# Kernel optimization log

Hardware: AMD Instinct MI355X
Metric: run time of the kernel (lower is better)

## Reference

```python
import jax, jax.numpy as jnp
import numpy as np

SEQ, B, IN, H, L = 256, 512, 300, 512, 256
EPS = 1e-5


def setup_inputs() -> dict:
    key = jax.random.key(0)
    ks = jax.random.split(key, 10)
    s_ih = 1.0 / np.sqrt(H)
    return {
        "x": jax.random.normal(ks[0], (SEQ, B, IN), dtype=jnp.float32),
        "W_ih": jax.random.normal(ks[1], (4 * H, IN), dtype=jnp.float32) * s_ih,
        "W_hh": jax.random.normal(ks[2], (4 * H, H), dtype=jnp.float32) * s_ih,
        "b_ih": jax.random.normal(ks[3], (4 * H,), dtype=jnp.float32) * s_ih,
        "b_hh": jax.random.normal(ks[4], (4 * H,), dtype=jnp.float32) * s_ih,
        "bn1_gamma": jnp.ones((H,), dtype=jnp.float32),
        "bn1_beta": jnp.zeros((H,), dtype=jnp.float32),
        "W1": jax.random.normal(ks[5], (L, H), dtype=jnp.float32) / np.sqrt(H),
        "b1": jax.random.normal(ks[6], (L,), dtype=jnp.float32) * 0.01,
        "bn2_gamma": jnp.ones((L,), dtype=jnp.float32),
        "bn2_beta": jnp.zeros((L,), dtype=jnp.float32),
        "W2": jax.random.normal(ks[7], (1, L), dtype=jnp.float32) / np.sqrt(L),
        "b2": jax.random.normal(ks[8], (1,), dtype=jnp.float32) * 0.01,
    }


def _batchnorm(x, gamma, beta):
    # training-mode BatchNorm1d: batch statistics, biased variance
    mean = jnp.mean(x, axis=0)
    var = jnp.var(x, axis=0)
    return (x - mean) * jax.lax.rsqrt(var + EPS) * gamma + beta


def reference(x, W_ih, W_hh, b_ih, b_hh, bn1_gamma, bn1_beta, W1, b1,
              bn2_gamma, bn2_beta, W2, b2):
    # Pre-compute the input projection for all timesteps in one big GEMM:
    # [S, B, IN] @ [IN, 4H] -> [S, B, 4H]
    x_proj = jnp.einsum('sbi,gi->sbg', x, W_ih) + b_ih + b_hh

    def step(carry, xt):
        h, c = carry
        gates = xt + h @ W_hh.T  # [B, 4H]
        i, f, g, o = jnp.split(gates, 4, axis=-1)
        i = jax.nn.sigmoid(i)
        f = jax.nn.sigmoid(f)
        g = jnp.tanh(g)
        o = jax.nn.sigmoid(o)
        c = f * c + i * g
        h = o * jnp.tanh(c)
        return (h, c), None

    h0 = jnp.zeros((x.shape[1], H), dtype=x.dtype)
    c0 = jnp.zeros((x.shape[1], H), dtype=x.dtype)
    (h, _c), _ = jax.lax.scan(step, (h0, c0), x_proj)
    # dropout with training=False -> identity

    h = _batchnorm(h, bn1_gamma, bn1_beta)
    h = h @ W1.T + b1
    h = _batchnorm(h, bn2_gamma, bn2_beta)
    h = jax.nn.relu(h)
    out = h @ W2.T + b2            # [B, 1]
    out = 4.0 * jax.nn.sigmoid(out)
    return out.squeeze(-1)         # [B]
```

## Files before the change

kernel.cpp:

```cpp
#include <hip/hip_runtime.h>
#include <math.h>

constexpr int SEQ   = 256;
constexpr int BATCH = 512;
constexpr int INDIM = 300;
constexpr int KIH   = 320;
constexpr int HDIM  = 512;
constexpr int LDIM  = 256;
constexpr int G4    = 4 * HDIM;

typedef _Float16 f16x8 __attribute__((ext_vector_type(8)));
typedef _Float16 f16x4 __attribute__((ext_vector_type(4)));
typedef float    f32x4 __attribute__((ext_vector_type(4)));


__global__ __launch_bounds__(256) void prep_weights_kernel(
    const float* __restrict__ Wih, const float* __restrict__ Whh,
    const float* __restrict__ bih, const float* __restrict__ bhh,
    _Float16* __restrict__ slab, float* __restrict__ bsum)
{
    const int by = blockIdx.x >> 6;
    const int rl = blockIdx.x & 63;
    const int g  = rl >> 4, r = rl & 15;
    const int grow = g * HDIM + by * 16 + r;
    const int tid = threadIdx.x;
    if (tid < 208) {
        const int col0 = tid * 4;
        f16x4 v;
        #pragma unroll
        for (int e = 0; e < 4; ++e) {
            const int col = col0 + e;
            float f;
            if (col < KIH) f = (col < INDIM) ? Wih[(size_t)grow * INDIM + col] : 0.f;
            else           f = Whh[(size_t)grow * HDIM + (col - KIH)];
            v[e] = (_Float16)f;
        }
        *(f16x4*)(slab + ((size_t)(by * 64 + rl)) * 832 + col0) = v;
    } else if (tid == 208) {
        bsum[grow] = bih[grow] + bhh[grow];
    }
}

__global__ __launch_bounds__(256) void prep_x_kernel(
    const float* __restrict__ x, _Float16* __restrict__ xall)
{
    const int rowl = threadIdx.x >> 6;
    const int s    = threadIdx.x & 63;
    const int row  = blockIdx.x * 4 + rowl;
    if (s >= 40) return;
    const int k0 = s * 8;
    const float* xr = x + (size_t)row * INDIM;
    f16x8 v;
    #pragma unroll
    for (int e = 0; e < 8; ++e)
        v[e] = (k0 + e < INDIM) ? (_Float16)xr[k0 + e] : (_Float16)0.f;
    *(f16x8*)(xall + (size_t)row * KIH + k0) = v;
}

__global__ __launch_bounds__(512, 2) void lstm_persist11(
    const _Float16* __restrict__ xall,
    const _Float16* __restrict__ slab,
    _Float16* __restrict__ hb,
    float* __restrict__ h32,
    const float* __restrict__ bsum,
    int* __restrict__ cnt)
{
    __shared__ _Float16 act[13][64][64];
    __shared__ float    Gb2[2][64][68];

    const int tid  = threadIdx.x;
    const int wid  = tid >> 6;
    const int lane = tid & 63;
    const int gg   = wid >> 2;
    const int bh   = (wid >> 1) & 1;
    const int ks   = wid & 1;
    const int l15  = lane & 15;
    const int q4   = lane >> 4;
    const int bx   = blockIdx.x & 7;
    const int by   = blockIdx.x >> 3;
    const int b0   = bx * 64;
    const int hc0  = by * 16;

    f16x8 ws[13][2];
    {
        const _Float16* sb = slab + (size_t)by * 64 * 832
                                  + (size_t)(gg * 32 + l15) * 832 + ks * 32 + q4 * 8;
        #pragma unroll
        for (int ch = 0; ch < 13; ++ch)
            #pragma unroll
            for (int mt = 0; mt < 2; ++mt) {
                const unsigned long long* p = (const unsigned long long*)
                    (sb + (size_t)mt * 16 * 832 + ch * 64);
                union { unsigned long long u[2]; f16x8 v; } w;
                w.u[0] = __hip_atomic_load(p,     __ATOMIC_RELAXED,
                                           __HIP_MEMORY_SCOPE_AGENT);
                w.u[1] = __hip_atomic_load(p + 1, __ATOMIC_RELAXED,
                                           __HIP_MEMORY_SCOPE_AGENT);
                ws[ch][mt] = w.v;
            }
    }

    const int srow  = tid >> 3;
    const int suu   = tid & 7;
    const int wbyte = srow * 128 + ((suu ^ (srow & 7)) << 4);

    int rbyte[2];
    #pragma unroll
    for (int bt = 0; bt < 2; ++bt) {
        const int row  = bh * 32 + bt * 16 + l15;
        const int unit = ks * 4 + q4;
        rbyte[bt] = row * 128 + ((unit ^ (row & 7)) << 4);
    }

    const int bl  = tid >> 3;
    const int j0l = (tid & 7) * 2;
    const int bg  = b0 + bl;
    const int jg  = hc0 + j0l;
    float bsv[4][2];
    #pragma unroll
    for (int g = 0; g < 4; ++g) {
        bsv[g][0] = bsum[g * HDIM + jg];
        bsv[g][1] = bsum[g * HDIM + jg + 1];
    }
    float cv0 = 0.f, cv1 = 0.f;

#define BARX() do { asm volatile("" ::: "memory");                           \
                    __builtin_amdgcn_s_barrier();                            \
                    asm volatile("" ::: "memory"); } while (0)
#define LGKM0() asm volatile("s_waitcnt lgkmcnt(0)" ::: "memory")
#define VM0()   asm volatile("s_waitcnt vmcnt(0)" ::: "memory")

#define MFMA_CHUNK(CH) do {                                                  \
        const char* base = (const char*)&act[CH][0][0];                      \
        const f16x8 bf0 = *(const f16x8*)(base + rbyte[0]);                  \
        const f16x8 bf1 = *(const f16x8*)(base + rbyte[1]);                  \
        acc00 = __builtin_amdgcn_mfma_f32_16x16x32_f16(ws[CH][0], bf0, acc00, 0, 0, 0); \
        acc01 = __builtin_amdgcn_mfma_f32_16x16x32_f16(ws[CH][0], bf1, acc01, 0, 0, 0); \
        acc10 = __builtin_amdgcn_mfma_f32_16x16x32_f16(ws[CH][1], bf0, acc10, 0, 0, 0); \
        acc11 = __builtin_amdgcn_mfma_f32_16x16x32_f16(ws[CH][1], bf1, acc11, 0, 0, 0); \
    } while (0)

    const _Float16* xpt = xall + (size_t)(b0 + srow) * KIH + suu * 8;
    const _Float16* hpt = hb + (size_t)(b0 + srow) * HDIM + suu * 8;

    f16x8 xcur[5], xnxt[5];
    #pragma unroll
    for (int ch = 0; ch < 5; ++ch)
        xcur[ch] = *(const f16x8*)(xpt + ch * 64);

    for (int t = 0; t < SEQ; ++t) {
        #pragma unroll
        for (int ch = 0; ch < 5; ++ch)
            *(f16x8*)((char*)&act[ch][0][0] + wbyte) = xcur[ch];
        LGKM0(); BARX();

        f32x4 acc00 = {0.f,0.f,0.f,0.f}, acc01 = {0.f,0.f,0.f,0.f};
        f32x4 acc10 = {0.f,0.f,0.f,0.f}, acc11 = {0.f,0.f,0.f,0.f};

        if (wid == 0) {
            if (t > 0) {
                const int* fp = cnt + bx * 32 + (lane & 31);
                int wd = 0;
                for (;;) {
                    const int f = __hip_atomic_load(fp, __ATOMIC_RELAXED,
                                                    __HIP_MEMORY_SCOPE_AGENT);
                    if (__all(f >= t)) break;
                    if (++wd > (1 << 20)) break;
                    __builtin_amdgcn_s_sleep(2);
                }
                asm volatile("" ::: "memory");
            }
        } else {
            MFMA_CHUNK(0); MFMA_CHUNK(1); MFMA_CHUNK(2);
            MFMA_CHUNK(3); MFMA_CHUNK(4);
        }
        BARX();

        f16x8 hr[8];
        {
            const _Float16* hbase = hpt + (size_t)(t & 1) * BATCH * HDIM;
            #pragma unroll
            for (int j = 0; j < 8; ++j) {
                const unsigned long long* p = (const unsigned long long*)
                    (hbase + j * 64);
                union { unsigned long long u[2]; f16x8 v; } hv;
                hv.u[0] = __hip_atomic_load(p,     __ATOMIC_RELAXED,
                                            __HIP_MEMORY_SCOPE_AGENT);
                hv.u[1] = __hip_atomic_load(p + 1, __ATOMIC_RELAXED,
                                            __HIP_MEMORY_SCOPE_AGENT);
                hr[j] = hv.v;
            }
        }
        if (wid == 0) {
            MFMA_CHUNK(0); MFMA_CHUNK(1); MFMA_CHUNK(2);
            MFMA_CHUNK(3); MFMA_CHUNK(4);
        }
        {
            const _Float16* xnb = xpt + (size_t)(t + 1) * BATCH * KIH;
            #pragma unroll
            for (int ch = 0; ch < 5; ++ch)
                xnxt[ch] = *(const f16x8*)(xnb + ch * 64);
        }
        #pragma unroll
        for (int j = 0; j < 8; ++j)
            *(f16x8*)((char*)&act[5 + j][0][0] + wbyte) = hr[j];
        LGKM0(); BARX();

        MFMA_CHUNK(5); MFMA_CHUNK(6); MFMA_CHUNK(7); MFMA_CHUNK(8);
        MFMA_CHUNK(9); MFMA_CHUNK(10); MFMA_CHUNK(11); MFMA_CHUNK(12);

        #pragma unroll
        for (int q = 0; q < 4; ++q) {
            Gb2[ks][gg * 32 +      q4 * 4 + q][bh * 32 +      l15] = acc00[q];
            Gb2[ks][gg * 32 +      q4 * 4 + q][bh * 32 + 16 + l15] = acc01[q];
            Gb2[ks][gg * 32 + 16 + q4 * 4 + q][bh * 32 +      l15] = acc10[q];
            Gb2[ks][gg * 32 + 16 + q4 * 4 + q][bh * 32 + 16 + l15] = acc11[q];
        }
        LGKM0(); BARX();

        {
            float pre[4][2];
            #pragma unroll
            for (int g = 0; g < 4; ++g) {
                pre[g][0] = Gb2[0][g * 16 + j0l    ][bl]
                          + Gb2[1][g * 16 + j0l    ][bl] + bsv[g][0];
                pre[g][1] = Gb2[0][g * 16 + j0l + 1][bl]
                          + Gb2[1][g * 16 + j0l + 1][bl] + bsv[g][1];
            }
            float hv0, hv1;
            {
                float vi = 1.f / (1.f + __expf(-pre[0][0]));
                float vf = 1.f / (1.f + __expf(-pre[1][0]));
                float vg = 1.f - 2.f / (__expf(2.f * pre[2][0]) + 1.f);
                float vo = 1.f / (1.f + __expf(-pre[3][0]));
                const float cc = vf * cv0 + vi * vg;
                cv0 = cc;
                hv0 = vo * (1.f - 2.f / (__expf(2.f * cc) + 1.f));
            }
            {
                float vi = 1.f / (1.f + __expf(-pre[0][1]));
                float vf = 1.f / (1.f + __expf(-pre[1][1]));
                float vg = 1.f - 2.f / (__expf(2.f * pre[2][1]) + 1.f);
                float vo = 1.f / (1.f + __expf(-pre[3][1]));
                const float cc = vf * cv1 + vi * vg;
                cv1 = cc;
                hv1 = vo * (1.f - 2.f / (__expf(2.f * cc) + 1.f));
            }
            union { unsigned int u; _Float16 v[2]; } hu;
            hu.v[0] = (_Float16)hv0; hu.v[1] = (_Float16)hv1;
            _Float16* hbw = hb + (size_t)((t + 1) & 1) * BATCH * HDIM;
            __hip_atomic_store((unsigned int*)(hbw + (size_t)bg * HDIM + jg),
                               hu.u, __ATOMIC_RELAXED, __HIP_MEMORY_SCOPE_AGENT);
            if (t == SEQ - 1) {
                float* hp = h32 + (size_t)bg * HDIM + jg;
                hp[0] = hv0; hp[1] = hv1;
            }
        }
        VM0(); BARX();
        if (tid == 0)
            __hip_atomic_store(&cnt[bx * 32 + by], t + 1, __ATOMIC_RELAXED,
                               __HIP_MEMORY_SCOPE_AGENT);

        #pragma unroll
        for (int ch = 0; ch < 5; ++ch) xcur[ch] = xnxt[ch];
    }
#undef BARX
#undef LGKM0
#undef VM0
#undef MFMA_CHUNK
}

__global__ __launch_bounds__(256) void prep_kernel(
    const float* __restrict__ Wih, const float* __restrict__ Whh,
    const float* __restrict__ bih, const float* __restrict__ bhh,
    _Float16* __restrict__ Wihc, _Float16* __restrict__ Whhc,
    float* __restrict__ bsum)
{
    const int g = blockIdx.x;
    for (int col = threadIdx.x; col < KIH; col += 256)
        Wihc[(size_t)g * KIH + col] =
            (col < INDIM) ? (_Float16)Wih[(size_t)g * INDIM + col] : (_Float16)0.f;
    for (int col = threadIdx.x; col < HDIM; col += 256)
        Whhc[(size_t)g * HDIM + col] = (_Float16)Whh[(size_t)g * HDIM + col];
    if (threadIdx.x == 0) bsum[g] = bih[g] + bhh[g];
}

__global__ __launch_bounds__(256) void fused_step_kernel(
    const float* __restrict__ xt, const _Float16* __restrict__ Wihc,
    const _Float16* __restrict__ Whhc, const float* __restrict__ bsum,
    float* __restrict__ c, float* __restrict__ h)
{
    __shared__ _Float16 As[32][72];
    __shared__ _Float16 Bs[128][72];
    __shared__ float    Gb[4][32][36];

    const int tid = threadIdx.x;
    const int b0  = blockIdx.x * 32;
    const int hc0 = blockIdx.y * 32;
    const int wid  = tid >> 6;
    const int lane = tid & 63;

    f32x4 acc[2][2] = {};
    const int arow = tid >> 3;
    const int ac8  = (tid & 7) * 8;
    const int brr  = tid >> 1;
    const int bseg = (tid & 1) * 32;

    for (int phase = 0; phase < 2; ++phase) {
        const float* Asrc = phase ? h : xt;
        const _Float16* Bsrc = phase ? Whhc : Wihc;
        const int Kpad = phase ? HDIM : KIH;
        const int Kval = phase ? HDIM : INDIM;
        const int astr = phase ? HDIM : INDIM;

        for (int k0 = 0; k0 < Kpad; k0 += 64) {
            const int gk = k0 + ac8;
            const float* pa = Asrc + (size_t)(b0 + arow) * astr + gk;
            float4 u = {0.f,0.f,0.f,0.f}, v = {0.f,0.f,0.f,0.f};
            if (gk + 3 < Kval)  u = *(const float4*)pa;
            if (gk + 7 < Kval)  v = *(const float4*)(pa + 4);
            f16x8 a8;
            a8[0]=(_Float16)u.x; a8[1]=(_Float16)u.y; a8[2]=(_Float16)u.z; a8[3]=(_Float16)u.w;
            a8[4]=(_Float16)v.x; a8[5]=(_Float16)v.y; a8[6]=(_Float16)v.z; a8[7]=(_Float16)v.w;
            const int grow = (brr >> 5) * HDIM + hc0 + (brr & 31);
            const _Float16* pb = Bsrc + (size_t)grow * Kpad + k0 + bseg;
            f16x8 w0 = *(const f16x8*)(pb + 0);
            f16x8 w1 = *(const f16x8*)(pb + 8);
            f16x8 w2 = *(const f16x8*)(pb + 16);
            f16x8 w3 = *(const f16x8*)(pb + 24);
            __syncthreads();
            *(f16x8*)&As[arow][ac8] = a8;
            *(f16x8*)&Bs[brr][bseg + 0]  = w0;
            *(f16x8*)&Bs[brr][bseg + 8]  = w1;
            *(f16x8*)&Bs[brr][bseg + 16] = w2;
            *(f16x8*)&Bs[brr][bseg + 24] = w3;
            __syncthreads();
            const int lr = lane & 15;
            const int lk = (lane >> 4) * 8;
            #pragma unroll
            for (int kf = 0; kf < 2; ++kf) {
                const int kl = kf * 32 + lk;
                f16x8 a0 = *(const f16x8*)&As[lr][kl];
                f16x8 a1 = *(const f16x8*)&As[16 + lr][kl];
                f16x8 bb0 = *(const f16x8*)&Bs[wid * 32 + lr][kl];
                f16x8 bb1 = *(const f16x8*)&Bs[wid * 32 + 16 + lr][kl];
                acc[0][0] = __builtin_amdgcn_mfma_f32_16x16x32_f16(a0, bb0, acc[0][0], 0, 0, 0);
                acc[0][1] = __builtin_amdgcn_mfma_f32_16x16x32_f16(a0, bb1, acc[0][1], 0, 0, 0);
                acc[1][0] = __builtin_amdgcn_mfma_f32_16x16x32_f16(a1, bb0, acc[1][0], 0, 0, 0);
                acc[1][1] = __builtin_amdgcn_mfma_f32_16x16x32_f16(a1, bb1, acc[1][1], 0, 0, 0);
            }
        }
    }
    __syncthreads();
    {
        const int cn = lane & 15;
        const int rbq = (lane >> 4) * 4;
        #pragma unroll
        for (int mi = 0; mi < 2; ++mi)
            #pragma unroll
            for (int ni = 0; ni < 2; ++ni)
                #pragma unroll
                for (int r = 0; r < 4; ++r)
                    Gb[wid][mi * 16 + rbq + r][ni * 16 + cn] = acc[mi][ni][r];
    }
    __syncthreads();
    {
        const int bl  = tid >> 3;
        const int jl0 = (tid & 7) * 4;
        const int gb  = b0 + bl;
        const int gj  = hc0 + jl0;
        const f32x4 ig = *(const f32x4*)&Gb[0][bl][jl0];
        const f32x4 fg = *(const f32x4*)&Gb[1][bl][jl0];
        const f32x4 gg = *(const f32x4*)&Gb[2][bl][jl0];
        const f32x4 og = *(const f32x4*)&Gb[3][bl][jl0];
        const f32x4 bi = *(const f32x4*)&bsum[0 * HDIM + gj];
        const f32x4 bf = *(const f32x4*)&bsum[1 * HDIM + gj];
        const f32x4 bg = *(const f32x4*)&bsum[2 * HDIM + gj];
        const f32x4 bo = *(const f32x4*)&bsum[3 * HDIM + gj];
        float* cp = c + (size_t)gb * HDIM + gj;
        float* hp = h + (size_t)gb * HDIM + gj;
        f32x4 cvv = *(const f32x4*)cp;
        f32x4 hv;
        #pragma unroll
        for (int q = 0; q < 4; ++q) {
            const float iv = 1.f / (1.f + __expf(-(ig[q] + bi[q])));
            const float fv = 1.f / (1.f + __expf(-(fg[q] + bf[q])));
            const float gv = tanhf(gg[q] + bg[q]);
            const float ov = 1.f / (1.f + __expf(-(og[q] + bo[q])));
            const float cc = fv * cvv[q] + iv * gv;
            cvv[q] = cc;
            hv[q] = ov * tanhf(cc);
        }
        *(f32x4*)cp = cvv;
        *(f32x4*)hp = hv;
    }
}

__global__ __launch_bounds__(256) void bn_stats_kernel(
    const float* __restrict__ X, int nfeat,
    const float* __restrict__ gamma, const float* __restrict__ beta,
    float* __restrict__ s, float* __restrict__ t)
{
    const int f = blockIdx.x * 256 + threadIdx.x;
    if (f >= nfeat) return;
    float sum = 0.f, sq = 0.f;
    for (int b = 0; b < BATCH; ++b) {
        const float v = X[(size_t)b * nfeat + f];
        sum += v; sq += v * v;
    }
    const float mean = sum * (1.f / BATCH);
    const float var  = sq * (1.f / BATCH) - mean * mean;
    const float rstd = rsqrtf(var + 1e-5f);
    const float sc   = gamma[f] * rstd;
    s[f] = sc;
    t[f] = beta[f] - mean * sc;
}

__global__ __launch_bounds__(256) void fc1_kernel(
    const float* __restrict__ h, const float* __restrict__ s1,
    const float* __restrict__ t1, const float* __restrict__ W1,
    const float* __restrict__ b1, float* __restrict__ out1)
{
    const int b = blockIdx.x;
    const int l = threadIdx.x;
    const float* hbp = h  + (size_t)b * HDIM;
    const float* wl  = W1 + (size_t)l * HDIM;
    float acc = 0.f;
    for (int k = 0; k < HDIM; ++k)
        acc += (hbp[k] * s1[k] + t1[k]) * wl[k];
    out1[(size_t)b * LDIM + l] = acc + b1[l];
}

__global__ __launch_bounds__(256) void final_kernel(
    const float* __restrict__ out1, const float* __restrict__ s2,
    const float* __restrict__ t2, const float* __restrict__ W2,
    const float* __restrict__ b2, float* __restrict__ out)
{
    const int b = blockIdx.x;
    float v = out1[(size_t)b * LDIM + threadIdx.x];
    v = v * s2[threadIdx.x] + t2[threadIdx.x];
    v = fmaxf(v, 0.f);
    v *= W2[threadIdx.x];
    #pragma unroll
    for (int off = 32; off > 0; off >>= 1) v += __shfl_down(v, off);
    __shared__ float red[4];
    if ((threadIdx.x & 63) == 0) red[threadIdx.x >> 6] = v;
    __syncthreads();
    if (threadIdx.x == 0) {
        const float ssum = red[0] + red[1] + red[2] + red[3] + b2[0];
        out[b] = 4.f / (1.f + expf(-ssum));
    }
}

extern "C" void kernel_launch(void* const* d_in, const int* in_sizes, int n_in,
                              void* d_out, int out_size, void* d_ws, size_t ws_size,
                              hipStream_t stream) {
    const float* x   = (const float*)d_in[0];
    const float* Wih = (const float*)d_in[1];
    const float* Whh = (const float*)d_in[2];
    const float* bih = (const float*)d_in[3];
    const float* bhh = (const float*)d_in[4];
    const float* g1  = (const float*)d_in[5];
    const float* be1 = (const float*)d_in[6];
    const float* W1  = (const float*)d_in[7];
    const float* b1  = (const float*)d_in[8];
    const float* g2  = (const float*)d_in[9];
    const float* be2 = (const float*)d_in[10];
    const float* W2  = (const float*)d_in[11];
    const float* b2  = (const float*)d_in[12];
    float* out = (float*)d_out;

    const size_t SZ_XALL = (size_t)(SEQ + 1) * BATCH * KIH * 2;
    const size_t SZ_SLAB = (size_t)32 * 64 * 832 * 2;
    const size_t SZ_HB   = (size_t)2 * BATCH * HDIM * 2;
    const size_t SZ_H32  = (size_t)BATCH * HDIM * 4;
    const size_t SZ_BSUM = (size_t)G4 * 4;
    const size_t SZ_CNT  = (size_t)SEQ * 8 * 4;
    const size_t SZ_ST   = (size_t)(HDIM * 2 + LDIM * 2) * 4;
    const size_t SZ_OUT1 = (size_t)BATCH * LDIM * 4;
    const size_t NEED = SZ_XALL + SZ_SLAB + SZ_HB + SZ_H32 + SZ_BSUM +
                        SZ_CNT + SZ_ST + SZ_OUT1;

    if (ws_size >= NEED) {
        char* p = (char*)d_ws;
        _Float16* xall = (_Float16*)p;           p += SZ_XALL;
        _Float16* slab = (_Float16*)p;           p += SZ_SLAB;
        _Float16* hbuf = (_Float16*)p;           p += SZ_HB;
        float* h32     = (float*)p;              p += SZ_H32;
        float* bsum    = (float*)p;              p += SZ_BSUM;
        int*   cnt     = (int*)p;                p += SZ_CNT;
        float* s1 = (float*)p;                   p += HDIM * 4;
        float* t1 = (float*)p;                   p += HDIM * 4;
        float* s2 = (float*)p;                   p += LDIM * 4;
        float* t2 = (float*)p;                   p += LDIM * 4;
        float* out1 = (float*)p;

        hipMemsetAsync(hbuf, 0, SZ_HB, stream);
        hipMemsetAsync(cnt, 0, SZ_CNT, stream);
        prep_weights_kernel<<<2048, 256, 0, stream>>>(Wih, Whh, bih, bhh, slab, bsum);
        prep_x_kernel<<<SEQ * 128, 256, 0, stream>>>(x, xall);

        lstm_persist11<<<dim3(256), dim3(512), 0, stream>>>(
            xall, slab, hbuf, h32, bsum, cnt);

        bn_stats_kernel<<<2, 256, 0, stream>>>(h32, HDIM, g1, be1, s1, t1);
        fc1_kernel<<<BATCH, 256, 0, stream>>>(h32, s1, t1, W1, b1, out1);
        bn_stats_kernel<<<1, 256, 0, stream>>>(out1, LDIM, g2, be2, s2, t2);
        final_kernel<<<BATCH, 256, 0, stream>>>(out1, s2, t2, W2, b2, out);
    } else {
        float* ws   = (float*)d_ws;
        float* h    = ws;
        float* c    = h + BATCH * HDIM;
        float* bsum = c + BATCH * HDIM;
        float* s1   = bsum + G4;
        float* t1   = s1 + HDIM;
        float* s2   = t1 + HDIM;
        float* t2   = s2 + LDIM;
        float* out1 = t2 + LDIM;
        _Float16* Wihc = (_Float16*)(out1 + (size_t)BATCH * LDIM);
        _Float16* Whhc = Wihc + (size_t)G4 * KIH;

        hipMemsetAsync(h, 0, (size_t)2 * BATCH * HDIM * sizeof(float), stream);
        prep_kernel<<<G4, 256, 0, stream>>>(Wih, Whh, bih, bhh, Wihc, Whhc, bsum);
        const dim3 sgrid(BATCH / 32, HDIM / 32);
        for (int t = 0; t < SEQ; ++t) {
            fused_step_kernel<<<sgrid, 256, 0, stream>>>(
                x + (size_t)t * BATCH * INDIM, Wihc, Whhc, bsum, c, h);
        }
        bn_stats_kernel<<<2, 256, 0, stream>>>(h, HDIM, g1, be1, s1, t1);
        fc1_kernel<<<BATCH, 256, 0, stream>>>(h, s1, t1, W1, b1, out1);
        bn_stats_kernel<<<1, 256, 0, stream>>>(out1, LDIM, g2, be2, s2, t2);
        final_kernel<<<BATCH, 256, 0, stream>>>(out1, s2, t2, W2, b2, out);
    }
}
```

Measured before the change: 1.281 ms.

## Split recurrent h wait and load into four quarter-pipelined stages

Instead of one wave waiting on all 32 producer flags before any h load, every wave now waits on 8 flags at a time, loads and stages that quarter of h into shared memory, and runs MFMAs on the previous quarter while waiting for the next. The aim is to overlap the cross-block synchronisation latency with the recurrent matmul, so work can start as soon as part of h_t is published. The cost is more block barriers per step (four instead of two), all waves polling global flags, and a shorter sleep, which adds memory traffic and barrier overhead.

```diff
diff --git a/kernel.cpp b/kernel.cpp
--- a/kernel.cpp
+++ b/kernel.cpp
@@ -57,7 +57,7 @@
     *(f16x8*)(xall + (size_t)row * KIH + k0) = v;
 }
 
-__global__ __launch_bounds__(512, 2) void lstm_persist11(
+__global__ __launch_bounds__(512, 2) void lstm_persist12(
     const _Float16* __restrict__ xall,
     const _Float16* __restrict__ slab,
     _Float16* __restrict__ hb,
@@ -140,6 +140,40 @@
         acc11 = __builtin_amdgcn_mfma_f32_16x16x32_f16(ws[CH][1], bf1, acc11, 0, 0, 0); \
     } while (0)
 
+#define WAITQ(G) do {                                                        \
+    if (t > 0) {                                                             \
+        const int* fp = cnt + bx * 32 + (G) * 8 + (lane & 7);                \
+        int wd = 0;                                                          \
+        for (;;) {                                                           \
+            const int f = __hip_atomic_load(fp, __ATOMIC_RELAXED,            \
+                                            __HIP_MEMORY_SCOPE_AGENT);      \
+            if (__all(f >= t)) break;                                        \
+            if (++wd > (1 << 20)) break;                                     \
+            __builtin_amdgcn_s_sleep(1);                                     \
+        }                                                                    \
+        asm volatile("" ::: "memory");                                       \
+    } } while (0)
+
+#define LOADG(G) do {                                                        \
+    _Pragma("unroll")                                                        \
+    for (int jj = 0; jj < 2; ++jj) {                                         \
+        const unsigned long long* p = (const unsigned long long*)            \
+            (hbase + ((G) * 2 + jj) * 64);                                   \
+        union { unsigned long long u[2]; f16x8 v; } hv;                      \
+        hv.u[0] = __hip_atomic_load(p,     __ATOMIC_RELAXED,                 \
+                                    __HIP_MEMORY_SCOPE_AGENT);              \
+        hv.u[1] = __hip_atomic_load(p + 1, __ATOMIC_RELAXED,                 \
+                                    __HIP_MEMORY_SCOPE_AGENT);              \
+        hr[(G) & 1][jj] = hv.v;                                              \
+    } } while (0)
+
+#define STAGEG(G) do {                                                       \
+    _Pragma("unroll")                                                        \
+    for (int jj = 0; jj < 2; ++jj)                                           \
+        *(f16x8*)((char*)&act[5 + (G) * 2 + jj][0][0] + wbyte)               \
+            = hr[(G) & 1][jj];                                               \
+    } while (0)
+
     const _Float16* xpt = xall + (size_t)(b0 + srow) * KIH + suu * 8;
     const _Float16* hpt = hb + (size_t)(b0 + srow) * HDIM + suu * 8;
 
@@ -149,6 +183,9 @@
         xcur[ch] = *(const f16x8*)(xpt + ch * 64);
 
     for (int t = 0; t < SEQ; ++t) {
+        const _Float16* hbase = hpt + (size_t)(t & 1) * BATCH * HDIM;
+        f16x8 hr[2][2];
+
         #pragma unroll
         for (int ch = 0; ch < 5; ++ch)
             *(f16x8*)((char*)&act[ch][0][0] + wbyte) = xcur[ch];
@@ -157,57 +194,27 @@
         f32x4 acc00 = {0.f,0.f,0.f,0.f}, acc01 = {0.f,0.f,0.f,0.f};
         f32x4 acc10 = {0.f,0.f,0.f,0.f}, acc11 = {0.f,0.f,0.f,0.f};
 
-        if (wid == 0) {
-            if (t > 0) {
-                const int* fp = cnt + bx * 32 + (lane & 31);
-                int wd = 0;
-                for (;;) {
-                    const int f = __hip_atomic_load(fp, __ATOMIC_RELAXED,
-                                                    __HIP_MEMORY_SCOPE_AGENT);
-                    if (__all(f >= t)) break;
-                    if (++wd > (1 << 20)) break;
-                    __builtin_amdgcn_s_sleep(2);
-                }
-                asm volatile("" ::: "memory");
-            }
-        } else {
-            MFMA_CHUNK(0); MFMA_CHUNK(1); MFMA_CHUNK(2);
-            MFMA_CHUNK(3); MFMA_CHUNK(4);
-        }
-        BARX();
-
-        f16x8 hr[8];
-        {
-            const _Float16* hbase = hpt + (size_t)(t & 1) * BATCH * HDIM;
-            #pragma unroll
-            for (int j = 0; j < 8; ++j) {
-                const unsigned long long* p = (const unsigned long long*)
-                    (hbase + j * 64);
-                union { unsigned long long u[2]; f16x8 v; } hv;
-                hv.u[0] = __hip_atomic_load(p,     __ATOMIC_RELAXED,
-                                            __HIP_MEMORY_SCOPE_AGENT);
-                hv.u[1] = __hip_atomic_load(p + 1, __ATOMIC_RELAXED,
-                                            __HIP_MEMORY_SCOPE_AGENT);
-                hr[j] = hv.v;
-            }
-        }
-        if (wid == 0) {
-            MFMA_CHUNK(0); MFMA_CHUNK(1); MFMA_CHUNK(2);
-            MFMA_CHUNK(3); MFMA_CHUNK(4);
-        }
+        MFMA_CHUNK(0); MFMA_CHUNK(1); MFMA_CHUNK(2);
+        MFMA_CHUNK(3); MFMA_CHUNK(4);
         {
             const _Float16* xnb = xpt + (size_t)(t + 1) * BATCH * KIH;
             #pragma unroll
             for (int ch = 0; ch < 5; ++ch)
                 xnxt[ch] = *(const f16x8*)(xnb + ch * 64);
         }
-        #pragma unroll
-        for (int j = 0; j < 8; ++j)
-            *(f16x8*)((char*)&act[5 + j][0][0] + wbyte) = hr[j];
-        LGKM0(); BARX();
-
-        MFMA_CHUNK(5); MFMA_CHUNK(6); MFMA_CHUNK(7); MFMA_CHUNK(8);
-        MFMA_CHUNK(9); MFMA_CHUNK(10); MFMA_CHUNK(11); MFMA_CHUNK(12);
+
+        WAITQ(0); LOADG(0);
+        STAGEG(0); LGKM0(); BARX();
+        WAITQ(1); LOADG(1);
+        MFMA_CHUNK(5); MFMA_CHUNK(6);
+        STAGEG(1); LGKM0(); BARX();
+        WAITQ(2); LOADG(2);
+        MFMA_CHUNK(7); MFMA_CHUNK(8);
+        STAGEG(2); LGKM0(); BARX();
+        WAITQ(3); LOADG(3);
+        MFMA_CHUNK(9); MFMA_CHUNK(10);
+        STAGEG(3); LGKM0(); BARX();
+        MFMA_CHUNK(11); MFMA_CHUNK(12);
 
         #pragma unroll
         for (int q = 0; q < 4; ++q) {
@@ -268,6 +275,9 @@
 #undef LGKM0
 #undef VM0
 #undef MFMA_CHUNK
+#undef WAITQ
+#undef LOADG
+#undef STAGEG
 }
 
 __global__ __launch_bounds__(256) void prep_kernel(
@@ -500,7 +510,7 @@
         prep_weights_kernel<<<2048, 256, 0, stream>>>(Wih, Whh, bih, bhh, slab, bsum);
         prep_x_kernel<<<SEQ * 128, 256, 0, stream>>>(x, xall);
 
-        lstm_persist11<<<dim3(256), dim3(512), 0, stream>>>(
+        lstm_persist12<<<dim3(256), dim3(512), 0, stream>>>(
             xall, slab, hbuf, h32, bsum, cnt);
 
         bn_stats_kernel<<<2, 256, 0, stream>>>(h32, HDIM, g1, be1, s1, t1);
```

Result: slower. 1.511 ms (+17.9%).
